# Performance work log

Measured on AMD Instinct MI355X. Metric: run time of the kernel, lower is better.

The kernel has to match this reference:

```python
import jax, jax.numpy as jnp
import numpy as np

EPS = 1e-6
SCAL = 5.0
PARTS = 16
NFEAT = 32
RES = 64


def conv(x, w, b, stride=1):
    y = jax.lax.conv_general_dilated(x, w, (stride, stride), 'SAME',
                                     dimension_numbers=('NCHW', 'OIHW', 'NCHW'))
    return y + b[None, :, None, None]


def spatial_softmax(x):
    b, k, h, w = x.shape
    return jax.nn.softmax(x.reshape(b, k, h * w), axis=-1).reshape(b, k, h, w)


def make_grid(h, w):
    ys = jnp.linspace(-1.0, 1.0, h)
    xs = jnp.linspace(-1.0, 1.0, w)
    gy, gx = jnp.meshgrid(ys, xs, indexing='ij')
    return jnp.stack([gy, gx], axis=-1)  # [h, w, 2]


def e_sigma(x, w1, b1, w2, b2, wp, bp):
    # shared shape/appearance encoder: parts via spatial softmax + residual sum map
    h1 = jax.nn.relu(conv(x, w1, b1, stride=2))   # [B,64,64,64]
    h2 = jax.nn.relu(conv(h1, w2, b2))            # [B,64,64,64]
    parts = spatial_softmax(conv(h2, wp, bp))     # [B,16,64,64]
    return parts, h2


def e_alpha(x, w1, b1, w2, b2):
    h1 = jax.nn.relu(conv(x, w1, b1))
    return conv(h1, w2, b2)                       # [B,32,64,64]


def get_mu_and_prec(parts):
    # soft-argmax mean + 2x2 covariance -> inverse Cholesky factor L_inv
    b, k, h, w = parts.shape
    grid = make_grid(h, w)
    mu = jnp.einsum('bkhw,hwc->bkc', parts, grid)                       # [b,k,2]
    outer = jnp.einsum('hwm,hwn->hwmn', grid, grid)
    cov = jnp.einsum('bkhw,hwmn->bkmn', parts, outer) - jnp.einsum('bkm,bkn->bkmn', mu, mu)
    a = jnp.sqrt(cov[..., 0, 0] + EPS)
    bb = cov[..., 0, 1] / (a + EPS)
    c = jnp.sqrt(jnp.maximum(cov[..., 1, 1] - bb * bb, 0.0) + EPS)
    det = a * c
    z = jnp.zeros_like(a)
    L_inv = SCAL / (det[..., None, None] + EPS) * jnp.stack(
        [jnp.stack([c, z], axis=-1), jnp.stack([-bb, a], axis=-1)], axis=-2)  # [b,k,2,2]
    return mu, L_inv


def feat_mu_to_enc(alpha, mu, L_inv, h, w):
    # render Cauchy-shaped part heatmaps from (mu, L_inv) and paint part features
    grid = make_grid(h, w)
    dist = grid[None, None] - mu[:, :, None, None, :]        # [b,k,h,w,2]
    proj = jnp.einsum('bkhwi,bkij->bkhwj', dist, L_inv)
    heat = 1.0 / (1.0 + jnp.sum(proj * proj, axis=-1))       # [b,k,h,w]
    norm = heat / (jnp.sum(heat, axis=(2, 3), keepdims=True) + EPS)
    fmap = jnp.einsum('bkf,bkhw->bfhw', alpha, norm)         # [b,nf,h,w]
    return jnp.concatenate([heat, fmap], axis=1)             # [b,nk+nf,h,w]


def decoder(enc, w1, b1, w2, b2, w3, b3):
    h1 = jax.nn.relu(conv(enc, w1, b1))                      # [B,64,64,64]
    up = jnp.repeat(jnp.repeat(h1, 2, axis=2), 2, axis=3)    # nearest upsample -> 128
    h2 = jax.nn.relu(conv(up, w2, b2))
    return jax.nn.sigmoid(conv(h2, w3, b3))                  # [B,3,128,128]


def setup_inputs():
    key = jax.random.key(0)
    ks = jax.random.split(key, 16)
    def w(k, shape):
        fan_in = shape[1] * shape[2] * shape[3]
        return (jax.random.normal(k, shape, jnp.float32) / np.sqrt(fan_in)).astype(jnp.float32)
    B = 32
    return {
        'x': jax.random.uniform(ks[0], (B, 3, 128, 128), jnp.float32),
        'x_spatial_transform': jax.random.uniform(ks[1], (B, 3, 128, 128), jnp.float32),
        'x_appearance_transform': jax.random.uniform(ks[2], (B, 3, 128, 128), jnp.float32),
        'coord': jax.random.normal(ks[3], (B, PARTS, 2), jnp.float32) * 0.5,
        'vector': jax.random.normal(ks[4], (B, PARTS, 2), jnp.float32) * 0.1,
        'es_w1': w(ks[5], (RES, 3, 3, 3)), 'es_b1': jnp.zeros((RES,), jnp.float32),
        'es_w2': w(ks[6], (RES, RES, 3, 3)), 'es_b2': jnp.zeros((RES,), jnp.float32),
        'es_wp': w(ks[7], (PARTS, RES, 3, 3)), 'es_bp': jnp.zeros((PARTS,), jnp.float32),
        'ea_w1': w(ks[8], (RES, RES, 3, 3)), 'ea_b1': jnp.zeros((RES,), jnp.float32),
        'ea_w2': w(ks[9], (NFEAT, RES, 3, 3)), 'ea_b2': jnp.zeros((NFEAT,), jnp.float32),
        'd_w1': w(ks[10], (RES, PARTS + NFEAT, 3, 3)), 'd_b1': jnp.zeros((RES,), jnp.float32),
        'd_w2': w(ks[11], (32, RES, 3, 3)), 'd_b2': jnp.zeros((32,), jnp.float32),
        'd_w3': w(ks[12], (3, 32, 3, 3)), 'd_b3': jnp.zeros((3,), jnp.float32),
    }


def reference(x, x_spatial_transform, x_appearance_transform, coord, vector,
              es_w1, es_b1, es_w2, es_b2, es_wp, es_bp,
              ea_w1, ea_b1, ea_w2, ea_b2,
              d_w1, d_b1, d_w2, d_b2, d_w3, d_b3):
    # shape stream (appearance-transformed image -> geometry)
    shape_parts, _ = e_sigma(x_appearance_transform, es_w1, es_b1, es_w2, es_b2, es_wp, es_bp)
    mu, L_inv = get_mu_and_prec(shape_parts)
    # appearance stream (spatially-transformed image -> appearance)
    app_parts, app_sum = e_sigma(x_spatial_transform, es_w1, es_b1, es_w2, es_b2, es_wp, es_bp)
    f_xs = e_alpha(app_sum, ea_w1, ea_b1, ea_w2, ea_b2)
    # local part appearances: gather features under each part map
    alpha = jnp.einsum('bfhw,bkhw->bkf', f_xs, app_parts)
    encoding = feat_mu_to_enc(alpha, mu, L_inv, 64, 64)
    reconstruction = decoder(encoding, d_w1, d_b1, d_w2, d_b2, d_w3, d_b3)
    # composite loss
    mu_a, L_inv_a = get_mu_and_prec(app_parts)
    rec_loss = jnp.mean((x - reconstruction) ** 2)
    equiv_loss = jnp.mean((mu - mu_a) ** 2) + 0.01 * jnp.mean((L_inv - L_inv_a) ** 2)
    transport_loss = jnp.mean((mu_a - (coord + vector)) ** 2)
    loss = rec_loss + equiv_loss + transport_loss
    return reconstruction, loss
```

## Files before the change

### kernel.cpp

```cpp
#include <hip/hip_runtime.h>
#include <hip/hip_bf16.h>

#define EPS 1e-6f
#define SCAL 5.0f

typedef __attribute__((ext_vector_type(8))) short bf8v;
typedef __attribute__((ext_vector_type(4))) float f32x4;

#define OFF_MU     0
#define OFF_LINV   1024
#define OFF_MUA    3072
#define OFF_LINVA  4096
#define OFF_HSUM   6144
#define OFF_ALPHA  6656
#define OFF_REC    23040
#define OFF_R1     32768
#define OFF_R2     (OFF_R1 + 8388608)
#define OFF_R3     (OFF_R2 + 8388608)
#define WS_TOTAL   (OFF_R3 + 16777216)

#define BA_XA   ((size_t)2 * OFF_R3)
#define BA_X2   ((size_t)2 * OFF_R1)
#define OFF_PARTSF OFF_R2
#define OFF_PROBS  (OFF_R2 + 4194304)
#define BA_EA1  ((size_t)2 * OFF_R3)
#define OFF_FXS (OFF_R3 + 4194304)
#define BA_E    ((size_t)2 * OFF_R2)
#define BA_D1   ((size_t)2 * OFF_R1)
#define BA_D2   ((size_t)2 * OFF_R3)

#define WT_ESW1 0
#define WT_ESB1 1728
#define WT_ESB2 1792
#define WT_ESBP 1856
#define WT_EAB1 1872
#define WT_EAB2 1936
#define WT_DB1  1968
#define WT_DB2  2032
#define WT_W3P  2064
#define WT_DB3  2928
#define P_WP2  0
#define P_WPP  36864
#define P_WPA1 46080
#define P_WPA2 82944
#define P_WPD1 101376
#define P_WPD2 138240

__device__ __attribute__((aligned(16))) float g_ws[WS_TOTAL];
__device__ __attribute__((aligned(16))) float g_wt[3072];
__device__ __attribute__((aligned(16))) __hip_bfloat16 g_wp[156672];
__device__ int g_isbf16;

__device__ __forceinline__ float selz(bool c, float v) { return c ? v : 0.f; }
__device__ __forceinline__ float cvtbf(short s) {
    return __uint_as_float(((unsigned int)(unsigned short)s) << 16);
}
__device__ __forceinline__ short f2bf(float f) {
    unsigned u = __float_as_uint(f);
    u += 0x7fff + ((u >> 16) & 1);
    return (short)(u >> 16);
}
__device__ __forceinline__ float ldin(const void* p, size_t i, int bf) {
    return bf ? __bfloat162float(((const __hip_bfloat16*)p)[i])
              : ((const float*)p)[i];
}

__device__ __forceinline__ float block_sum(float v) {
    __shared__ float sb[8];
    for (int off = 32; off; off >>= 1) v += __shfl_down(v, off, 64);
    int lane = threadIdx.x & 63, wid = threadIdx.x >> 6;
    __syncthreads();
    if (lane == 0) sb[wid] = v;
    __syncthreads();
    float r = 0.f;
    for (int i = 0; i < 4; ++i) r += sb[i];
    return r;
}
__device__ __forceinline__ float block_max(float v) {
    __shared__ float sb[8];
    for (int off = 32; off; off >>= 1) v = fmaxf(v, __shfl_down(v, off, 64));
    int lane = threadIdx.x & 63, wid = threadIdx.x >> 6;
    __syncthreads();
    if (lane == 0) sb[wid] = v;
    __syncthreads();
    float r = -1e30f;
    for (int i = 0; i < 4; ++i) r = fmaxf(r, sb[i]);
    return r;
}

__global__ void detect_k(const void* x) {
    const __hip_bfloat16* p = (const __hip_bfloat16*)x;
    int lane = threadIdx.x & 63;
    float v = 0.f;
    for (int i = lane; i < 256; i += 64) {
        float a = fabsf(__bfloat162float(p[i]));
        if (!(a <= 2.0f)) v = 1.f;
    }
    for (int off = 32; off; off >>= 1) v += __shfl_down(v, off, 64);
    if (lane == 0) {
        g_isbf16 = (v == 0.f) ? 1 : 0;
        g_ws[OFF_REC] = 0.f;
    }
}

__global__ void wpack_k(const void* esw1, const void* esb1, const void* esw2, const void* esb2,
                        const void* eswp, const void* esbp, const void* eaw1, const void* eab1,
                        const void* eaw2, const void* eab2, const void* dw1, const void* db1,
                        const void* dw2, const void* db2, const void* dw3, const void* db3) {
    int bf = g_isbf16;
    int gid0 = blockIdx.x * 256 + threadIdx.x, stride = gridDim.x * 256;
    for (int g = gid0; g < 512; g += stride) g_ws[OFF_HSUM + g] = 0.f;
    for (int g = gid0; g < 1728; g += stride) g_wt[WT_ESW1 + g] = ldin(esw1, g, bf);
    for (int g = gid0; g < 64; g += stride) g_wt[WT_ESB1 + g] = ldin(esb1, g, bf);
    for (int g = gid0; g < 64; g += stride) g_wt[WT_ESB2 + g] = ldin(esb2, g, bf);
    for (int g = gid0; g < 16; g += stride) g_wt[WT_ESBP + g] = ldin(esbp, g, bf);
    for (int g = gid0; g < 64; g += stride) g_wt[WT_EAB1 + g] = ldin(eab1, g, bf);
    for (int g = gid0; g < 32; g += stride) g_wt[WT_EAB2 + g] = ldin(eab2, g, bf);
    for (int g = gid0; g < 64; g += stride) g_wt[WT_DB1 + g] = ldin(db1, g, bf);
    for (int g = gid0; g < 32; g += stride) g_wt[WT_DB2 + g] = ldin(db2, g, bf);
    for (int g = gid0; g < 3; g += stride) g_wt[WT_DB3 + g] = ldin(db3, g, bf);
    for (int g = gid0; g < 864; g += stride) {
        int t = g / 96, o = (g / 32) % 3, k = g & 31;
        g_wt[WT_W3P + g] = ldin(dw3, (size_t)(o * 32 + k) * 9 + t, bf);
    }
    for (int g = gid0; g < 36864; g += stride) {
        int kk = g & 31, n = (g >> 5) & 63, tc = g >> 11;
        int t = tc >> 1, k = (tc & 1) * 32 + kk;
        g_wp[P_WP2 + g] = __float2bfloat16(ldin(esw2, (size_t)(n * 64 + k) * 9 + t, bf));
    }
    for (int g = gid0; g < 9216; g += stride) {
        int kk = g & 31, n = (g >> 5) & 15, tc = g >> 9;
        int t = tc >> 1, k = (tc & 1) * 32 + kk;
        g_wp[P_WPP + g] = __float2bfloat16(ldin(eswp, (size_t)(n * 64 + k) * 9 + t, bf));
    }
    for (int g = gid0; g < 36864; g += stride) {
        int kk = g & 31, n = (g >> 5) & 63, tc = g >> 11;
        int t = tc >> 1, k = (tc & 1) * 32 + kk;
        g_wp[P_WPA1 + g] = __float2bfloat16(ldin(eaw1, (size_t)(n * 64 + k) * 9 + t, bf));
    }
    for (int g = gid0; g < 18432; g += stride) {
        int kk = g & 31, n = (g >> 5) & 31, tc = g >> 10;
        int t = tc >> 1, k = (tc & 1) * 32 + kk;
        g_wp[P_WPA2 + g] = __float2bfloat16(ldin(eaw2, (size_t)(n * 64 + k) * 9 + t, bf));
    }
    for (int g = gid0; g < 36864; g += stride) {
        int kk = g & 31, n = (g >> 5) & 63, tc = g >> 11;
        int t = tc >> 1, k = (tc & 1) * 32 + kk;
        float v = (k < 48) ? ldin(dw1, (size_t)(n * 48 + k) * 9 + t, bf) : 0.f;
        g_wp[P_WPD1 + g] = __float2bfloat16(v);
    }
    for (int g = gid0; g < 18432; g += stride) {
        int kk = g & 31, n = (g >> 5) & 31, tc = g >> 10;
        int t = tc >> 1, k = (tc & 1) * 32 + kk;
        g_wp[P_WPD2 + g] = __float2bfloat16(ldin(dw2, (size_t)(n * 64 + k) * 9 + t, bf));
    }
}

__global__ void __launch_bounds__(256)
conv_s2n_k(const void* __restrict__ inA, const void* __restrict__ inB) {
    int bf = g_isbf16;
    int tile = blockIdx.x & 15;
    int b = blockIdx.x >> 4;
    const void* in = (b < 32) ? inA : inB;
    int bb = b & 31;
    int pix = tile * 256 + threadIdx.x;
    int y = pix >> 6, x = pix & 63;
    size_t inb = (size_t)bb * 3 * 16384;
    float acc[64];
    #pragma unroll
    for (int o = 0; o < 64; ++o) acc[o] = g_wt[WT_ESB1 + o];
    int iy0 = 2 * y, ix0 = 2 * x;
    bool my2 = (iy0 + 2 < 128), mx2 = (ix0 + 2 < 128);
    int iy2 = my2 ? iy0 + 2 : 127, ix2 = mx2 ? ix0 + 2 : 127;
    for (int ic = 0; ic < 3; ++ic) {
        size_t pb = inb + ic * 16384;
        float t[9];
        t[0] = ldin(in, pb + iy0 * 128 + ix0, bf);
        t[1] = ldin(in, pb + iy0 * 128 + ix0 + 1, bf);
        t[2] = selz(mx2, ldin(in, pb + iy0 * 128 + ix2, bf));
        t[3] = ldin(in, pb + (iy0 + 1) * 128 + ix0, bf);
        t[4] = ldin(in, pb + (iy0 + 1) * 128 + ix0 + 1, bf);
        t[5] = selz(mx2, ldin(in, pb + (iy0 + 1) * 128 + ix2, bf));
        t[6] = selz(my2, ldin(in, pb + iy2 * 128 + ix0, bf));
        t[7] = selz(my2, ldin(in, pb + iy2 * 128 + ix0 + 1, bf));
        t[8] = selz(my2 && mx2, ldin(in, pb + iy2 * 128 + ix2, bf));
        #pragma unroll
        for (int o = 0; o < 64; ++o) {
            const float* wr = g_wt + WT_ESW1 + (o * 3 + ic) * 9;
            float a = acc[o];
            #pragma unroll
            for (int j = 0; j < 9; ++j) a = fmaf(t[j], wr[j], a);
            acc[o] = a;
        }
    }
    __hip_bfloat16* out = (__hip_bfloat16*)g_ws + BA_XA + ((size_t)b * 4096 + pix) * 64;
    #pragma unroll
    for (int o = 0; o < 64; ++o) out[o] = __float2bfloat16(fmaxf(acc[o], 0.f));
}

template<int TR>
__device__ __forceinline__ void stage_tile(__hip_bfloat16* sA,
                                           const __hip_bfloat16* __restrict__ inb, int y0) {
    for (int g = threadIdx.x; g < TR * 512; g += 256) {
        int r = g >> 9;
        int rem = g & 511;
        int px = rem >> 3, j = rem & 7;
        int yy = y0 - 1 + r;
        int P = px + 1;
        bf8v v = (bf8v){0, 0, 0, 0, 0, 0, 0, 0};
        if (yy >= 0 && yy <= 63)
            v = *(const bf8v*)(inb + ((size_t)(yy * 64 + px) * 64 + j * 8));
        *(bf8v*)(sA + ((r * 66 + P) * 64 + ((j ^ (P & 7)) * 8))) = v;
    }
    if (threadIdx.x < TR * 16) {
        int g = threadIdx.x;
        int r = g >> 4, rem = g & 15, side = rem >> 3, j = rem & 7;
        int P = side ? 65 : 0;
        *(bf8v*)(sA + ((r * 66 + P) * 64 + ((j ^ (P & 7)) * 8))) = (bf8v){0, 0, 0, 0, 0, 0, 0, 0};
    }
}

template<int MS>
__device__ __forceinline__ void ld_a(const __hip_bfloat16* sA, int it, int rowIn,
                                     int l15, int quad, bf8v (&a)[MS]) {
    const int t = it >> 1, c = it & 1;
    const int dy = t / 3 - 1, dx = t % 3 - 1;
    const int r = rowIn + 1 + dy;
    const int j = c * 4 + quad;
    #pragma unroll
    for (int ms = 0; ms < MS; ++ms) {
        int P = ms * 16 + l15 + dx + 1;
        a[ms] = *(const bf8v*)(sA + ((r * 66 + P) * 64 + ((j ^ (P & 7)) * 8)));
    }
}
template<int MS>
__device__ __forceinline__ void ld_a2(const __hip_bfloat16* sA, int it, int rowbase,
                                      int l15, int quad, bf8v (&a)[2][MS]) {
    const int t = it >> 1, c = it & 1;
    const int dy = t / 3 - 1, dx = t % 3 - 1;
    const int j = c * 4 + quad;
    #pragma unroll
    for (int rp = 0; rp < 2; ++rp) {
        const int r = rowbase + rp + 1 + dy;
        #pragma unroll
        for (int ms = 0; ms < MS; ++ms) {
            int P = ms * 16 + l15 + dx + 1;
            a[rp][ms] = *(const bf8v*)(sA + ((r * 66 + P) * 64 + ((j ^ (P & 7)) * 8)));
        }
    }
}
template<int TOTN, int NS>
__device__ __forceinline__ void ld_b(int it, int ocoff, int l15, int quad, int wp_off,
                                     bf8v (&bv)[NS]) {
    #pragma unroll
    for (int ns = 0; ns < NS; ++ns)
        bv[ns] = *(const bf8v*)(g_wp + wp_off +
                 ((size_t)(it * TOTN + ocoff + ns * 16 + l15) * 32 + quad * 8));
}

template<int TOTN, int NS, int MS>
__device__ __forceinline__ void conv_body(const __hip_bfloat16* sA, int rowIn,
                                          int l15, int quad, int wp_off,
                                          f32x4 (&acc)[MS][NS]) {
    bf8v bq[3][NS];
    bf8v a[2][MS];
    ld_b<TOTN, NS>(0, 0, l15, quad, wp_off, bq[0]);
    ld_b<TOTN, NS>(1, 0, l15, quad, wp_off, bq[1]);
    ld_a<MS>(sA, 0, rowIn, l15, quad, a[0]);
    #pragma unroll
    for (int it = 0; it < 18; ++it) {
        if (it + 2 < 18) ld_b<TOTN, NS>(it + 2, 0, l15, quad, wp_off, bq[(it + 2) % 3]);
        if (it + 1 < 18) ld_a<MS>(sA, it + 1, rowIn, l15, quad, a[(it + 1) & 1]);
        #pragma unroll
        for (int ns = 0; ns < NS; ++ns)
            #pragma unroll
            for (int ms = 0; ms < MS; ++ms)
                acc[ms][ns] = __builtin_amdgcn_mfma_f32_16x16x32_bf16(
                    a[it & 1][ms], bq[it % 3][ns], acc[ms][ns], 0, 0, 0);
    }
}

template<int TOTN, int NSW, int MS>
__device__ __forceinline__ void conv_body2(const __hip_bfloat16* sA, int rowbase, int ocoff,
                                           int l15, int quad, int wp_off,
                                           f32x4 (&acc)[2][MS][NSW]) {
    bf8v bq[3][NSW];
    bf8v a[2][2][MS];
    ld_b<TOTN, NSW>(0, ocoff, l15, quad, wp_off, bq[0]);
    ld_b<TOTN, NSW>(1, ocoff, l15, quad, wp_off, bq[1]);
    ld_a2<MS>(sA, 0, rowbase, l15, quad, a[0]);
    #pragma unroll
    for (int it = 0; it < 18; ++it) {
        if (it + 2 < 18) ld_b<TOTN, NSW>(it + 2, ocoff, l15, quad, wp_off, bq[(it + 2) % 3]);
        if (it + 1 < 18) ld_a2<MS>(sA, it + 1, rowbase, l15, quad, a[(it + 1) & 1]);
        #pragma unroll
        for (int rp = 0; rp < 2; ++rp)
            #pragma unroll
            for (int ns = 0; ns < NSW; ++ns)
                #pragma unroll
                for (int ms = 0; ms < MS; ++ms)
                    acc[rp][ms][ns] = __builtin_amdgcn_mfma_f32_16x16x32_bf16(
                        a[it & 1][rp][ms], bq[it % 3][ns], acc[rp][ms][ns], 0, 0, 0);
    }
}

template<int TOTN, int NSW, int OUTF32, int RELU>
__device__ __forceinline__ void epi_2r(f32x4 (&acc)[2][4][NSW], int bO, int y0, int rowbase,
                                       int ocoff, int l15, int quad, int bias_off,
                                       size_t out_off) {
    #pragma unroll
    for (int rp = 0; rp < 2; ++rp) {
        int y = y0 + rowbase + rp;
        #pragma unroll
        for (int ns = 0; ns < NSW; ++ns) {
            float bias = g_wt[bias_off + ocoff + ns * 16 + l15];
            #pragma unroll
            for (int ms = 0; ms < 4; ++ms) {
                #pragma unroll
                for (int r = 0; r < 4; ++r) {
                    int pix = ms * 16 + quad * 4 + r;
                    float v = acc[rp][ms][ns][r] + bias;
                    if (RELU) v = fmaxf(v, 0.f);
                    size_t o = out_off + ((size_t)(bO * 4096 + y * 64 + pix)) * TOTN +
                               ocoff + ns * 16 + l15;
                    if (OUTF32) g_ws[o] = v;
                    else ((__hip_bfloat16*)g_ws)[o] = __float2bfloat16(v);
                }
            }
        }
    }
}

template<int TOTN, int NSW, int OUTF32, int RELU>
__global__ void __launch_bounds__(256) __attribute__((amdgpu_waves_per_eu(2, 3)))
conv_mfl_k(size_t in_off, int wp_off, int bias_off, size_t out_off) {
    __shared__ __hip_bfloat16 sA[6 * 66 * 64];
    int wid = threadIdx.x >> 6, lane = threadIdx.x & 63;
    int l15 = lane & 15, quad = lane >> 4;
    int b = blockIdx.x >> 4, y0 = (blockIdx.x & 15) * 4;
    int og = wid & 1, rowbase = (wid >> 1) * 2;
    int ocoff = og * NSW * 16;
    const __hip_bfloat16* inb = (const __hip_bfloat16*)g_ws + in_off + (size_t)b * 4096 * 64;
    stage_tile<6>(sA, inb, y0);
    __syncthreads();
    f32x4 acc[2][4][NSW];
    #pragma unroll
    for (int rp = 0; rp < 2; ++rp)
        #pragma unroll
        for (int ms = 0; ms < 4; ++ms)
            #pragma unroll
            for (int ns = 0; ns < NSW; ++ns) acc[rp][ms][ns] = (f32x4){0.f, 0.f, 0.f, 0.f};
    conv_body2<TOTN, NSW, 4>(sA, rowbase, ocoff, l15, quad, wp_off, acc);
    epi_2r<TOTN, NSW, OUTF32, RELU>(acc, b, y0, rowbase, ocoff, l15, quad, bias_off, out_off);
}

__global__ void __launch_bounds__(256) __attribute__((amdgpu_waves_per_eu(2, 3)))
conv_pea_k() {
    __shared__ __hip_bfloat16 sA[6 * 66 * 64];
    int wid = threadIdx.x >> 6, lane = threadIdx.x & 63;
    int l15 = lane & 15, quad = lane >> 4;
    int b = blockIdx.x & 63;
    int y0 = (int)(blockIdx.x >> 6) * 4;
    const __hip_bfloat16* inb = (const __hip_bfloat16*)g_ws + BA_X2 + (size_t)b * 4096 * 64;
    stage_tile<6>(sA, inb, y0);
    __syncthreads();
    f32x4 accP[4][1];
    #pragma unroll
    for (int ms = 0; ms < 4; ++ms) accP[ms][0] = (f32x4){0.f, 0.f, 0.f, 0.f};
    conv_body<16, 1, 4>(sA, wid, l15, quad, P_WPP, accP);
    if (b >= 32) {
        int og = wid & 1, rowbase = (wid >> 1) * 2;
        int ocoff = og * 32;
        f32x4 accE[2][4][2];
        #pragma unroll
        for (int rp = 0; rp < 2; ++rp)
            #pragma unroll
            for (int ms = 0; ms < 4; ++ms)
                #pragma unroll
                for (int ns = 0; ns < 2; ++ns) accE[rp][ms][ns] = (f32x4){0.f, 0.f, 0.f, 0.f};
        conv_body2<64, 2, 4>(sA, rowbase, ocoff, l15, quad, P_WPA1, accE);
        epi_2r<64, 2, 0, 1>(accE, b - 32, y0, rowbase, ocoff, l15, quad, WT_EAB1, BA_EA1);
    }
    __syncthreads();
    float* tb = (float*)sA;
    float biasP = g_wt[WT_ESBP + l15];
    #pragma unroll
    for (int ms = 0; ms < 4; ++ms)
        #pragma unroll
        for (int r = 0; r < 4; ++r)
            tb[l15 * 260 + wid * 64 + ms * 16 + quad * 4 + r] = accP[ms][0][r] + biasP;
    __syncthreads();
    int k = threadIdx.x >> 4, xo = (threadIdx.x & 15) * 16;
    float* dst = g_ws + OFF_PARTSF + ((size_t)(b * 16 + k)) * 4096 + y0 * 64 + xo;
    const float* src = tb + k * 260 + xo;
    #pragma unroll
    for (int i = 0; i < 16; i += 4)
        *(f32x4*)(dst + i) = *(const f32x4*)(src + i);
}

__global__ void __launch_bounds__(256) __attribute__((amdgpu_waves_per_eu(2, 3)))
conv_upmf2_k(size_t in_off, int wp_off, int bias_off, size_t out_off) {
    __shared__ __hip_bfloat16 sA[4 * 66 * 64];
    int wid = threadIdx.x >> 6, lane = threadIdx.x & 63;
    int l15 = lane & 15, quad = lane >> 4;
    int b = blockIdx.x >> 5, y0 = (blockIdx.x & 31) * 4;
    int ri0 = (y0 >> 1) - 1;
    const __hip_bfloat16* inb = (const __hip_bfloat16*)g_ws + in_off + (size_t)b * 4096 * 64;
    for (int g = threadIdx.x; g < 2048; g += 256) {
        int r = g >> 9;
        int rem = g & 511;
        int px = rem >> 3, j = rem & 7;
        int yi = ri0 + r;
        int P = px + 1;
        bf8v v = (bf8v){0, 0, 0, 0, 0, 0, 0, 0};
        if (yi >= 0 && yi <= 63)
            v = *(const bf8v*)(inb + ((size_t)(yi * 64 + px) * 64 + j * 8));
        *(bf8v*)(sA + ((r * 66 + P) * 64 + ((j ^ (P & 7)) * 8))) = v;
    }
    if (threadIdx.x < 64) {
        int g = threadIdx.x;
        int r = g >> 4, rem = g & 15, side = rem >> 3, j = rem & 7;
        int P = side ? 65 : 0;
        *(bf8v*)(sA + ((r * 66 + P) * 64 + ((j ^ (P & 7)) * 8))) = (bf8v){0, 0, 0, 0, 0, 0, 0, 0};
    }
    __syncthreads();
    int og = wid & 1, rowbase = (wid >> 1) * 2;
    f32x4 acc[2][8];
    #pragma unroll
    for (int rp = 0; rp < 2; ++rp)
        #pragma unroll
        for (int ms = 0; ms < 8; ++ms) acc[rp][ms] = (f32x4){0.f, 0.f, 0.f, 0.f};
    bf8v bq[3][1];
    ld_b<32, 1>(0, og * 16, l15, quad, wp_off, bq[0]);
    ld_b<32, 1>(1, og * 16, l15, quad, wp_off, bq[1]);
    #pragma unroll
    for (int it = 0; it < 18; ++it) {
        if (it + 2 < 18) ld_b<32, 1>(it + 2, og * 16, l15, quad, wp_off, bq[(it + 2) % 3]);
        const int t = it >> 1, c = it & 1;
        const int dy = t / 3 - 1, dx = t % 3 - 1;
        #pragma unroll
        for (int rp = 0; rp < 2; ++rp) {
            int yy = y0 + rowbase + rp + dy;
            if (yy >= 0 && yy <= 127) {
                int r = (yy >> 1) - ri0;
                int j = c * 4 + quad;
                bf8v a[8];
                #pragma unroll
                for (int ms = 0; ms < 8; ++ms) {
                    int xx = ms * 16 + l15 + dx;
                    int P = (xx < 0) ? 0 : ((xx > 127) ? 65 : ((xx >> 1) + 1));
                    a[ms] = *(const bf8v*)(sA + ((r * 66 + P) * 64 + ((j ^ (P & 7)) * 8)));
                }
                #pragma unroll
                for (int ms = 0; ms < 8; ++ms)
                    acc[rp][ms] = __builtin_amdgcn_mfma_f32_16x16x32_bf16(a[ms], bq[it % 3][0], acc[rp][ms], 0, 0, 0);
            }
        }
    }
    float bias = g_wt[bias_off + og * 16 + l15];
    #pragma unroll
    for (int rp = 0; rp < 2; ++rp) {
        int y = y0 + rowbase + rp;
        #pragma unroll
        for (int ms = 0; ms < 8; ++ms) {
            #pragma unroll
            for (int r = 0; r < 4; ++r) {
                int pix = ms * 16 + quad * 4 + r;
                float v = fmaxf(acc[rp][ms][r] + bias, 0.f);
                size_t o = out_off + ((size_t)(b * 16384 + y * 128 + pix)) * 32 + og * 16 + l15;
                ((__hip_bfloat16*)g_ws)[o] = __float2bfloat16(v);
            }
        }
    }
}

__global__ void sm_mom3_k() {
    int bk = blockIdx.x;
    int b = bk >> 4;
    int app = (b >= 32);
    const float* P = g_ws + OFF_PARTSF + (size_t)bk * 4096;
    float r[16];
    #pragma unroll
    for (int j = 0; j < 16; ++j) r[j] = P[threadIdx.x + j * 256];
    float m = r[0];
    #pragma unroll
    for (int j = 1; j < 16; ++j) m = fmaxf(m, r[j]);
    m = block_max(m);
    float s = 0.f;
    #pragma unroll
    for (int j = 0; j < 16; ++j) { r[j] = __expf(r[j] - m); s += r[j]; }
    s = block_sum(s);
    float inv = 1.0f / s;
    float sy = 0, sx = 0, syy = 0, sxy = 0, sxx = 0;
    #pragma unroll
    for (int j = 0; j < 16; ++j) {
        float pv = r[j] * inv;
        int i = threadIdx.x + j * 256;
        if (app) g_ws[OFF_PROBS + (size_t)(bk - 512) * 4096 + i] = pv;
        float gy = -1.0f + (i >> 6) * (2.0f / 63.0f);
        float gx = -1.0f + (i & 63) * (2.0f / 63.0f);
        sy += pv * gy; sx += pv * gx;
        syy += pv * gy * gy; sxy += pv * gy * gx; sxx += pv * gx * gx;
    }
    sy = block_sum(sy); sx = block_sum(sx);
    syy = block_sum(syy); sxy = block_sum(sxy); sxx = block_sum(sxx);
    if (threadIdx.x == 0) {
        float c00 = syy - sy * sy, c01 = sxy - sy * sx, c11 = sxx - sx * sx;
        float a = sqrtf(fmaxf(c00 + EPS, 1e-12f));
        float bb = c01 / (a + EPS);
        float cc = sqrtf(fmaxf(c11 - bb * bb, 0.f) + EPS);
        float det = a * cc;
        float sc = SCAL / (det + EPS);
        int idx = app ? (bk - 512) : bk;
        int mu_off = app ? OFF_MUA : OFF_MU;
        int linv_off = app ? OFF_LINVA : OFF_LINV;
        g_ws[mu_off + idx * 2 + 0] = sy;
        g_ws[mu_off + idx * 2 + 1] = sx;
        g_ws[linv_off + idx * 4 + 0] = cc * sc;
        g_ws[linv_off + idx * 4 + 1] = 0.f;
        g_ws[linv_off + idx * 4 + 2] = -bb * sc;
        g_ws[linv_off + idx * 4 + 3] = a * sc;
    }
}

__global__ void alpha2_k() {
    int b = blockIdx.x & 31, k = blockIdx.x >> 5;
    int bk = b * 16 + k;
    __shared__ float pl[4096];
    const float* pr = g_ws + OFF_PROBS + (size_t)bk * 4096;
    for (int i = threadIdx.x; i < 4096; i += 256) pl[i] = pr[i];
    __syncthreads();
    float acc[32];
    #pragma unroll
    for (int f = 0; f < 32; ++f) acc[f] = 0.f;
    for (int i = threadIdx.x; i < 4096; i += 256) {
        float pv = pl[i];
        const float* fp = g_ws + OFF_FXS + (size_t)(b * 4096 + i) * 32;
        #pragma unroll
        for (int f = 0; f < 32; ++f) acc[f] = fmaf(pv, fp[f], acc[f]);
    }
    __shared__ float sw[4][32];
    int lane = threadIdx.x & 63, wid = threadIdx.x >> 6;
    #pragma unroll
    for (int f = 0; f < 32; ++f)
        for (int off = 32; off; off >>= 1) acc[f] += __shfl_down(acc[f], off, 64);
    if (lane == 0) {
        #pragma unroll
        for (int f = 0; f < 32; ++f) sw[wid][f] = acc[f];
    }
    __syncthreads();
    if (threadIdx.x < 32)
        g_ws[OFF_ALPHA + bk * 32 + threadIdx.x] =
            sw[0][threadIdx.x] + sw[1][threadIdx.x] + sw[2][threadIdx.x] + sw[3][threadIdx.x];
}

__global__ void heat2_k() {
    int tile = blockIdx.x & 15, b = blockIdx.x >> 4;
    __shared__ float hs[16];
    if (threadIdx.x < 16) hs[threadIdx.x] = 0.f;
    __syncthreads();
    int pix = tile * 256 + threadIdx.x;
    float gy = -1.0f + (pix >> 6) * (2.0f / 63.0f);
    float gx = -1.0f + (pix & 63) * (2.0f / 63.0f);
    bf8v e0, e1;
    float hv[16];
    #pragma unroll
    for (int k = 0; k < 16; ++k) {
        int bk = b * 16 + k;
        float m0 = g_ws[OFF_MU + bk * 2], m1 = g_ws[OFF_MU + bk * 2 + 1];
        float L00 = g_ws[OFF_LINV + bk * 4 + 0], L10 = g_ws[OFF_LINV + bk * 4 + 2],
              L11 = g_ws[OFF_LINV + bk * 4 + 3];
        float d0 = gy - m0, d1 = gx - m1;
        float p0 = d0 * L00 + d1 * L10;
        float p1 = d1 * L11;
        float h = 1.0f / (1.0f + p0 * p0 + p1 * p1);
        hv[k] = h;
        short sbits = f2bf(h);
        if (k < 8) e0[k] = sbits; else e1[k - 8] = sbits;
    }
    __hip_bfloat16* E = (__hip_bfloat16*)g_ws + BA_E + (size_t)(b * 4096 + pix) * 64;
    *(bf8v*)E = e0;
    *(bf8v*)(E + 8) = e1;
    #pragma unroll
    for (int k = 0; k < 16; ++k) {
        float v = hv[k];
        for (int off = 32; off; off >>= 1) v += __shfl_down(v, off, 64);
        if ((threadIdx.x & 63) == 0) atomicAdd(&hs[k], v);
    }
    __syncthreads();
    if (threadIdx.x < 16)
        atomicAdd(&g_ws[OFF_HSUM + b * 16 + threadIdx.x], hs[threadIdx.x]);
}

__global__ void fmap2_k() {
    int tile = blockIdx.x & 15, b = blockIdx.x >> 4;
    __shared__ float coef[16][32];
    for (int i = threadIdx.x; i < 512; i += 256) {
        int k = i >> 5, f = i & 31;
        coef[k][f] = g_ws[OFF_ALPHA + (b * 16 + k) * 32 + f] /
                     (g_ws[OFF_HSUM + b * 16 + k] + EPS);
    }
    __syncthreads();
    int pix = tile * 256 + threadIdx.x;
    __hip_bfloat16* E = (__hip_bfloat16*)g_ws + BA_E + (size_t)(b * 4096 + pix) * 64;
    float h[16];
    #pragma unroll
    for (int k = 0; k < 16; ++k) h[k] = __bfloat162float(E[k]);
    #pragma unroll
    for (int f = 0; f < 32; ++f) {
        float a = 0.f;
        #pragma unroll
        for (int k = 0; k < 16; ++k) a = fmaf(h[k], coef[k][f], a);
        E[16 + f] = __float2bfloat16(a);
    }
    #pragma unroll
    for (int z = 48; z < 64; ++z) E[z] = __float2bfloat16(0.f);
}

__device__ __forceinline__ void ld_tap9(const short* __restrict__ D2, int y, int x, int t,
                                        bf8v (&dst)[4]) {
    int dy = t / 3 - 1, dx = t % 3 - 1;
    int yy = y + dy, xx = x + dx;
    bool ok = ((unsigned)yy < 128u) && ((unsigned)xx < 128u);
    const short* sp = D2 + (size_t)((ok ? yy : y) * 128 + (ok ? xx : x)) * 32;
    const bf8v zv = (bf8v){0, 0, 0, 0, 0, 0, 0, 0};
    #pragma unroll
    for (int c = 0; c < 4; ++c) {
        bf8v tmp = *(const bf8v*)(sp + c * 8);
        dst[c] = ok ? tmp : zv;
    }
}
__device__ __forceinline__ void fma_tap(const bf8v (&v)[4], int t, float (&acc)[3]) {
    #pragma unroll
    for (int c = 0; c < 4; ++c)
        #pragma unroll
        for (int j = 0; j < 8; ++j) {
            float av = cvtbf(v[c][j]);
            int kk = c * 8 + j;
            acc[0] = fmaf(av, g_wt[WT_W3P + (t * 3 + 0) * 32 + kk], acc[0]);
            acc[1] = fmaf(av, g_wt[WT_W3P + (t * 3 + 1) * 32 + kk], acc[1]);
            acc[2] = fmaf(av, g_wt[WT_W3P + (t * 3 + 2) * 32 + kk], acc[2]);
        }
}
__global__ void __launch_bounds__(256)
conv_sign_k(const void* __restrict__ ximg, void* __restrict__ outp) {
    int bf = g_isbf16;
    int tile = blockIdx.x & 63, b = blockIdx.x >> 6;
    int pix = tile * 256 + threadIdx.x;
    int y = pix >> 7, x = pix & 127;
    const short* D2 = (const short*)((const __hip_bfloat16*)g_ws + BA_D2 + (size_t)b * 16384 * 32);
    float acc[3];
    #pragma unroll
    for (int o = 0; o < 3; ++o) acc[o] = g_wt[WT_DB3 + o];
    bf8v vA[4], vB[4];
    ld_tap9(D2, y, x, 0, vA);
    #pragma unroll 1
    for (int tt = 0; tt < 4; ++tt) {
        int t0 = 2 * tt, t1 = 2 * tt + 1;
        ld_tap9(D2, y, x, t1, vB);
        fma_tap(vA, t0, acc);
        ld_tap9(D2, y, x, t1 + 1, vA);
        fma_tap(vB, t1, acc);
    }
    fma_tap(vA, 8, acc);
    float es = 0.f;
    #pragma unroll
    for (int o = 0; o < 3; ++o) {
        float v = 1.0f / (1.0f + __expf(-acc[o]));
        size_t oidx = ((size_t)b * 3 + o) * 16384 + pix;
        if (bf) ((__hip_bfloat16*)outp)[oidx] = __float2bfloat16(v);
        else    ((float*)outp)[oidx] = v;
        float e = ldin(ximg, oidx, bf) - v;
        es += e * e;
    }
    float s = block_sum(es);
    if (threadIdx.x == 0) atomicAdd(&g_ws[OFF_REC], s);
}

__global__ void loss_k(const void* __restrict__ coord,
                       const void* __restrict__ vec,
                       void* __restrict__ outp) {
    int bf = g_isbf16;
    const float* mu = g_ws + OFF_MU;
    const float* linv = g_ws + OFF_LINV;
    const float* mu_a = g_ws + OFF_MUA;
    const float* linv_a = g_ws + OFF_LINVA;
    float s1 = 0, s2 = 0, s3 = 0;
    for (int i = threadIdx.x; i < 1024; i += 256) {
        float d = mu[i] - mu_a[i];
        s1 += d * d;
        float t = ldin(coord, i, bf) + ldin(vec, i, bf);
        float d3 = mu_a[i] - t;
        s3 += d3 * d3;
    }
    for (int i = threadIdx.x; i < 2048; i += 256) {
        float d = linv[i] - linv_a[i];
        s2 += d * d;
    }
    s1 = block_sum(s1);
    s2 = block_sum(s2);
    s3 = block_sum(s3);
    if (threadIdx.x == 0) {
        float loss = g_ws[OFF_REC] / 1572864.0f + s1 / 1024.0f + 0.01f * (s2 / 2048.0f)
                   + s3 / 1024.0f;
        if (bf) ((__hip_bfloat16*)outp)[1572864] = __float2bfloat16(loss);
        else    ((float*)outp)[1572864] = loss;
    }
}

extern "C" void kernel_launch(void* const* d_in, const int* in_sizes, int n_in,
                              void* d_out, int out_size, void* d_ws, size_t ws_size,
                              hipStream_t stream) {
    const void* x     = d_in[0];
    const void* x_st  = d_in[1];
    const void* x_at  = d_in[2];
    const void* coord = d_in[3];
    const void* vec   = d_in[4];

    dim3 blk(256);

    detect_k<<<1, 64, 0, stream>>>(x);
    wpack_k<<<64, blk, 0, stream>>>(
        d_in[5],  d_in[6],  d_in[7],  d_in[8],
        d_in[9],  d_in[10], d_in[11], d_in[12],
        d_in[13], d_in[14], d_in[15], d_in[16],
        d_in[17], d_in[18], d_in[19], d_in[20]);

    conv_s2n_k<<<64 * 16, blk, 0, stream>>>(x_at, x_st);
    conv_mfl_k<64, 2, 0, 1><<<1024, blk, 0, stream>>>(BA_XA, P_WP2, WT_ESB2, BA_X2);

    conv_pea_k<<<1024, blk, 0, stream>>>();
    sm_mom3_k<<<1024, blk, 0, stream>>>();

    conv_mfl_k<32, 1, 1, 0><<<512, blk, 0, stream>>>(BA_EA1, P_WPA2, WT_EAB2, (size_t)OFF_FXS);
    alpha2_k<<<512, blk, 0, stream>>>();

    heat2_k<<<512, blk, 0, stream>>>();
    fmap2_k<<<512, blk, 0, stream>>>();

    conv_mfl_k<64, 2, 0, 1><<<512, blk, 0, stream>>>(BA_E, P_WPD1, WT_DB1, BA_D1);
    conv_upmf2_k<<<1024, blk, 0, stream>>>(BA_D1, P_WPD2, WT_DB2, BA_D2);
    conv_sign_k<<<32 * 64, blk, 0, stream>>>(x, d_out);

    loss_k<<<1, blk, 0, stream>>>(coord, vec, d_out);
}
```

Baseline: 385.7 us.

## Stage final conv input rows plus halo in swizzled LDS

The final 3x3 conv (32->3 channels, sigmoid) now loads a 4-row halo tile of the 128-wide bf16 activation into shared memory with an XOR swizzle, then reads all nine taps from LDS instead of issuing nine sets of global loads per pixel. This removes the redundant global and L2 traffic from neighbouring pixels that re-read the same data. In exchange it adds about 33 KB of LDS per block and a __syncthreads, which may reduce occupancy. The conv is only one small stage of the whole pipeline.

```diff
diff --git a/kernel.cpp b/kernel.cpp
--- a/kernel.cpp
+++ b/kernel.cpp
@@ -617,52 +617,58 @@
     for (int z = 48; z < 64; ++z) E[z] = __float2bfloat16(0.f);
 }
 
-__device__ __forceinline__ void ld_tap9(const short* __restrict__ D2, int y, int x, int t,
-                                        bf8v (&dst)[4]) {
-    int dy = t / 3 - 1, dx = t % 3 - 1;
-    int yy = y + dy, xx = x + dx;
-    bool ok = ((unsigned)yy < 128u) && ((unsigned)xx < 128u);
-    const short* sp = D2 + (size_t)((ok ? yy : y) * 128 + (ok ? xx : x)) * 32;
-    const bf8v zv = (bf8v){0, 0, 0, 0, 0, 0, 0, 0};
-    #pragma unroll
-    for (int c = 0; c < 4; ++c) {
-        bf8v tmp = *(const bf8v*)(sp + c * 8);
-        dst[c] = ok ? tmp : zv;
-    }
-}
-__device__ __forceinline__ void fma_tap(const bf8v (&v)[4], int t, float (&acc)[3]) {
-    #pragma unroll
-    for (int c = 0; c < 4; ++c)
-        #pragma unroll
-        for (int j = 0; j < 8; ++j) {
-            float av = cvtbf(v[c][j]);
-            int kk = c * 8 + j;
-            acc[0] = fmaf(av, g_wt[WT_W3P + (t * 3 + 0) * 32 + kk], acc[0]);
-            acc[1] = fmaf(av, g_wt[WT_W3P + (t * 3 + 1) * 32 + kk], acc[1]);
-            acc[2] = fmaf(av, g_wt[WT_W3P + (t * 3 + 2) * 32 + kk], acc[2]);
-        }
-}
 __global__ void __launch_bounds__(256)
 conv_sign_k(const void* __restrict__ ximg, void* __restrict__ outp) {
+    __shared__ __hip_bfloat16 sD[4 * 66 * 64];
     int bf = g_isbf16;
-    int tile = blockIdx.x & 63, b = blockIdx.x >> 6;
-    int pix = tile * 256 + threadIdx.x;
-    int y = pix >> 7, x = pix & 127;
-    const short* D2 = (const short*)((const __hip_bfloat16*)g_ws + BA_D2 + (size_t)b * 16384 * 32);
+    int rp = blockIdx.x & 63, b = blockIdx.x >> 6;
+    int y0 = rp * 2;
+    const __hip_bfloat16* inb = (const __hip_bfloat16*)g_ws + BA_D2 + (size_t)b * 16384 * 32;
+    for (int g = threadIdx.x; g < 2048; g += 256) {
+        int r = g >> 9;
+        int rem = g & 511;
+        int px = rem >> 3, j = rem & 7;
+        int yy = y0 - 1 + r;
+        int P = px + 1;
+        bf8v v = (bf8v){0, 0, 0, 0, 0, 0, 0, 0};
+        if (yy >= 0 && yy <= 127)
+            v = *(const bf8v*)(inb + ((size_t)(yy * 128 + px * 2 + (j >> 2)) * 32 + (j & 3) * 8));
+        *(bf8v*)(sD + ((r * 66 + P) * 64 + ((j ^ (P & 7)) * 8))) = v;
+    }
+    if (threadIdx.x < 64) {
+        int g = threadIdx.x;
+        int r = g >> 4, rem = g & 15, side = rem >> 3, j = rem & 7;
+        int P = side ? 65 : 0;
+        *(bf8v*)(sD + ((r * 66 + P) * 64 + ((j ^ (P & 7)) * 8))) = (bf8v){0, 0, 0, 0, 0, 0, 0, 0};
+    }
+    __syncthreads();
+    int yloc = threadIdx.x >> 7;
+    int x = threadIdx.x & 127;
+    int pix = yloc * 128 + x + y0 * 128;
     float acc[3];
     #pragma unroll
     for (int o = 0; o < 3; ++o) acc[o] = g_wt[WT_DB3 + o];
-    bf8v vA[4], vB[4];
-    ld_tap9(D2, y, x, 0, vA);
-    #pragma unroll 1
-    for (int tt = 0; tt < 4; ++tt) {
-        int t0 = 2 * tt, t1 = 2 * tt + 1;
-        ld_tap9(D2, y, x, t1, vB);
-        fma_tap(vA, t0, acc);
-        ld_tap9(D2, y, x, t1 + 1, vA);
-        fma_tap(vB, t1, acc);
-    }
-    fma_tap(vA, 8, acc);
+    #pragma unroll
+    for (int t = 0; t < 9; ++t) {
+        int dy = t / 3 - 1, dx = t % 3 - 1;
+        int r = yloc + dy + 1;
+        int xs = x + dx;
+        int P = (xs >> 1) + 1;
+        int hw = xs & 1;
+        #pragma unroll
+        for (int c = 0; c < 4; ++c) {
+            int j = hw * 4 + c;
+            bf8v v = *(const bf8v*)(sD + ((r * 66 + P) * 64 + ((j ^ (P & 7)) * 8)));
+            #pragma unroll
+            for (int jj = 0; jj < 8; ++jj) {
+                float av = cvtbf(v[jj]);
+                int kk = c * 8 + jj;
+                acc[0] = fmaf(av, g_wt[WT_W3P + (t * 3 + 0) * 32 + kk], acc[0]);
+                acc[1] = fmaf(av, g_wt[WT_W3P + (t * 3 + 1) * 32 + kk], acc[1]);
+                acc[2] = fmaf(av, g_wt[WT_W3P + (t * 3 + 2) * 32 + kk], acc[2]);
+            }
+        }
+    }
     float es = 0.f;
     #pragma unroll
     for (int o = 0; o < 3; ++o) {
```

Result: slower. 449.0 us (+16.4%).
